# Optimization experiments

Hardware: AMD Instinct MI355X
Metric: run time of the kernel (lower is better)

Reference implementation:

```python
import jax, jax.numpy as jnp
import numpy as np

# Locally-connected 3D conv, channels_last, valid padding, stride 1
B, IX, IY, IZ, CIN = 4, 32, 32, 16, 8
KX, KY, KZ = 3, 3, 3
F = 8
OX, OY, OZ = IX - KX + 1, IY - KY + 1, IZ - KZ + 1  # 30, 30, 14
IN_SIZE = IX * IY * IZ * CIN
OUT_SIZE = OX * OY * OZ * F
NNZ = OX * OY * OZ * F * KX * KY * KZ * CIN  # 21,772,800


def _kernel_idxs():
    # rows/cols of the sparse (OUT_SIZE, IN_SIZE) locally-connected kernel
    # dim order: (ox, oy, oz, fo, kx, ky, kz, ci)
    ox = np.arange(OX).reshape(OX, 1, 1, 1, 1, 1, 1, 1)
    oy = np.arange(OY).reshape(1, OY, 1, 1, 1, 1, 1, 1)
    oz = np.arange(OZ).reshape(1, 1, OZ, 1, 1, 1, 1, 1)
    fo = np.arange(F).reshape(1, 1, 1, F, 1, 1, 1, 1)
    kx = np.arange(KX).reshape(1, 1, 1, 1, KX, 1, 1, 1)
    ky = np.arange(KY).reshape(1, 1, 1, 1, 1, KY, 1, 1)
    kz = np.arange(KZ).reshape(1, 1, 1, 1, 1, 1, KZ, 1)
    ci = np.arange(CIN).reshape(1, 1, 1, 1, 1, 1, 1, CIN)
    full = (OX, OY, OZ, F, KX, KY, KZ, CIN)
    row = ((ox * OY + oy) * OZ + oz) * F + fo
    col = (((ox + kx) * IY + (oy + ky)) * IZ + (oz + kz)) * CIN + ci
    rows = np.broadcast_to(row, full).ravel().astype(np.int32)
    cols = np.broadcast_to(col, full).ravel().astype(np.int32)
    return rows, cols


def setup_inputs() -> dict:
    key = jax.random.key(0)
    k = jax.random.split(key, 7)
    rows, cols = _kernel_idxs()
    inputs = jax.random.normal(k[0], (B, IX, IY, IZ, CIN), dtype=jnp.float32)
    kernel_mean = jax.random.normal(k[1], (NNZ,), dtype=jnp.float32) * 0.05
    # posterior stddev (positive), analogous to softplus(rho) in tfp mean-field posterior
    kernel_std = jax.nn.softplus(jax.random.normal(k[2], (NNZ,), dtype=jnp.float32) - 4.0)
    bias = jax.random.normal(k[3], (OX, OY, OZ, F), dtype=jnp.float32) * 0.05
    eps = jax.random.normal(k[4], (NNZ,), dtype=jnp.float32)
    sign_in = (2.0 * jax.random.bernoulli(k[5], 0.5, (B, IN_SIZE)).astype(jnp.float32) - 1.0)
    sign_out = (2.0 * jax.random.bernoulli(k[6], 0.5, (B, OUT_SIZE)).astype(jnp.float32) - 1.0)
    return {"inputs": inputs, "kernel_mean": kernel_mean, "kernel_std": kernel_std,
            "bias": bias, "eps": eps, "sign_in": sign_in, "sign_out": sign_out,
            "rows": jnp.asarray(rows), "cols": jnp.asarray(cols)}


def _local_conv(x_flat_T, kvals, rows, cols):
    # x_flat_T: [IN_SIZE, B]; sparse matmul: out[row, b] += kvals * x[col, b]
    contrib = kvals[:, None] * x_flat_T[cols]          # [NNZ, B]
    out = jax.ops.segment_sum(contrib, rows, num_segments=OUT_SIZE)  # [OUT_SIZE, B]
    return out.T                                        # [B, OUT_SIZE]


def reference(inputs, kernel_mean, kernel_std, bias, eps, sign_in, sign_out, rows, cols):
    x_flat = inputs.reshape(B, -1)                      # [B, IN_SIZE]
    mean_out = _local_conv(x_flat.T, kernel_mean, rows, cols)
    # flipout perturbation: sign_out * lc(x * sign_in, std * eps)
    pert = _local_conv((x_flat * sign_in).T, kernel_std * eps, rows, cols) * sign_out
    out = (mean_out + pert).reshape(B, OX, OY, OZ, F) + bias
    return out  # linear activation
```

## Files before the change

kernel.cpp:

```cpp
#include <hip/hip_runtime.h>


constexpr int B = 4, IX = 32, IY = 32, IZ = 16, CIN = 8;
constexpr int KX = 3, KY = 3, KZ = 3, F = 8;
constexpr int OX = IX - KX + 1;
constexpr int OY = IY - KY + 1;
constexpr int OZ = IZ - KZ + 1;
constexpr int IN_SIZE  = IX * IY * IZ * CIN;
constexpr int OUT_SIZE = OX * OY * OZ * F;
constexpr int TAPS = KX * KY * KZ * CIN;

__global__ __launch_bounds__(256, 4) void lc3d_flipout_kernel(
    const float* __restrict__ x,
    const float* __restrict__ kmean,
    const float* __restrict__ kstd,
    const float* __restrict__ bias,
    const float* __restrict__ eps,
    const float* __restrict__ sgn_in,
    const float* __restrict__ sgn_out,
    float* __restrict__ out)
{
    const int gtid = blockIdx.x * blockDim.x + threadIdx.x;
    const int o    = gtid >> 6;
    const int lane = threadIdx.x & 63;
    if (o >= OUT_SIZE) return;

    const int t  = o >> 3;
    const int oz = t % OZ;
    const int t2 = t / OZ;
    const int oy = t2 % OY;
    const int ox = t2 / OY;

    float ms0 = 0.f, ms1 = 0.f, ms2 = 0.f, ms3 = 0.f;
    float ps0 = 0.f, ps1 = 0.f, ps2 = 0.f, ps3 = 0.f;

    if (lane < TAPS / 4) {
        const int s   = lane >> 1;
        const int ci0 = (lane & 1) << 2;
        const int kz  = s % KZ;
        const int sy  = s / KZ;
        const int ky  = sy % KY;
        const int kx  = sy / KY;
        const int col = (((ox + kx) * IY + (oy + ky)) * IZ + (oz + kz)) * CIN + ci0;
        const int nb  = o * TAPS + (lane << 2);

        const float4 m4 = *reinterpret_cast<const float4*>(kmean + nb);
        const float4 s4 = *reinterpret_cast<const float4*>(kstd  + nb);
        const float4 e4 = *reinterpret_cast<const float4*>(eps   + nb);
        float4 se;
        se.x = s4.x * e4.x; se.y = s4.y * e4.y; se.z = s4.z * e4.z; se.w = s4.w * e4.w;

#define ACC_BATCH(bi, msv, psv)                                                     \
        {                                                                           \
            const float4 x4 = *reinterpret_cast<const float4*>(x + (bi)*IN_SIZE + col);      \
            const float4 si = *reinterpret_cast<const float4*>(sgn_in + (bi)*IN_SIZE + col); \
            msv += m4.x*x4.x + m4.y*x4.y + m4.z*x4.z + m4.w*x4.w;                   \
            psv += se.x*(x4.x*si.x) + se.y*(x4.y*si.y)                              \
                 + se.z*(x4.z*si.z) + se.w*(x4.w*si.w);                             \
        }
        ACC_BATCH(0, ms0, ps0)
        ACC_BATCH(1, ms1, ps1)
        ACC_BATCH(2, ms2, ps2)
        ACC_BATCH(3, ms3, ps3)
#undef ACC_BATCH
    }

#pragma unroll
    for (int off = 32; off >= 1; off >>= 1) {
        ms0 += __shfl_xor(ms0, off, 64);
        ms1 += __shfl_xor(ms1, off, 64);
        ms2 += __shfl_xor(ms2, off, 64);
        ms3 += __shfl_xor(ms3, off, 64);
        ps0 += __shfl_xor(ps0, off, 64);
        ps1 += __shfl_xor(ps1, off, 64);
        ps2 += __shfl_xor(ps2, off, 64);
        ps3 += __shfl_xor(ps3, off, 64);
    }

    if (lane < B) {
        const float m = (lane == 0) ? ms0 : (lane == 1) ? ms1 : (lane == 2) ? ms2 : ms3;
        const float p = (lane == 0) ? ps0 : (lane == 1) ? ps1 : (lane == 2) ? ps2 : ps3;
        out[lane * OUT_SIZE + o] = m + sgn_out[lane * OUT_SIZE + o] * p + bias[o];
    }
}

extern "C" void kernel_launch(void* const* d_in, const int* in_sizes, int n_in,
                              void* d_out, int out_size, void* d_ws, size_t ws_size,
                              hipStream_t stream) {
    const float* x       = (const float*)d_in[0];
    const float* kmean   = (const float*)d_in[1];
    const float* kstd    = (const float*)d_in[2];
    const float* bias    = (const float*)d_in[3];
    const float* eps     = (const float*)d_in[4];
    const float* sgn_in  = (const float*)d_in[5];
    const float* sgn_out = (const float*)d_in[6];
    float* out = (float*)d_out;

    const int waves   = OUT_SIZE;
    const int threads = 256;
    const int blocks  = (waves * 64 + threads - 1) / threads;

    hipLaunchKernelGGL(lc3d_flipout_kernel, dim3(blocks), dim3(threads), 0, stream,
                       x, kmean, kstd, bias, eps, sgn_in, sgn_out, out);
}
```

Baseline: 343.6 us.

## Map one wavefront per spatial position with all filters and XCD-aware block remap

```diff
diff --git a/kernel.cpp b/kernel.cpp
--- a/kernel.cpp
+++ b/kernel.cpp
@@ -9,8 +9,10 @@
 constexpr int IN_SIZE  = IX * IY * IZ * CIN;
 constexpr int OUT_SIZE = OX * OY * OZ * F;
 constexpr int TAPS = KX * KY * KZ * CIN;
+constexpr int NSPAT = OX * OY * OZ;
+constexpr int WROW = F * TAPS;
 
-__global__ __launch_bounds__(256, 4) void lc3d_flipout_kernel(
+__global__ __launch_bounds__(256, 4) void lc3d_flipout_v2(
     const float* __restrict__ x,
     const float* __restrict__ kmean,
     const float* __restrict__ kstd,
@@ -20,67 +22,74 @@
     const float* __restrict__ sgn_out,
     float* __restrict__ out)
 {
-    const int gtid = blockIdx.x * blockDim.x + threadIdx.x;
-    const int o    = gtid >> 6;
+    const int nwg = (NSPAT * 64) / 256;
+    const int q = nwg / 8, r = nwg % 8;
+    const int xcd = blockIdx.x % 8, idx = blockIdx.x / 8;
+    const int bid = (xcd < r ? xcd * (q + 1) : r * (q + 1) + (xcd - r) * q) + idx;
+
+    const int wid  = (bid * 256 + (int)threadIdx.x) >> 6;
     const int lane = threadIdx.x & 63;
-    if (o >= OUT_SIZE) return;
+    const int fo = lane >> 3;
+    const int g  = lane & 7;
+    const int sp = wid;
+    if (sp >= NSPAT) return;
 
-    const int t  = o >> 3;
-    const int oz = t % OZ;
-    const int t2 = t / OZ;
+    const int oz = sp % OZ;
+    const int t2 = sp / OZ;
     const int oy = t2 % OY;
     const int ox = t2 / OY;
+    const int obase = sp * F;
 
-    float ms0 = 0.f, ms1 = 0.f, ms2 = 0.f, ms3 = 0.f;
-    float ps0 = 0.f, ps1 = 0.f, ps2 = 0.f, ps3 = 0.f;
+    float ms[4] = {0.f, 0.f, 0.f, 0.f};
+    float ps[4] = {0.f, 0.f, 0.f, 0.f};
 
-    if (lane < TAPS / 4) {
-        const int s   = lane >> 1;
-        const int ci0 = (lane & 1) << 2;
-        const int kz  = s % KZ;
-        const int sy  = s / KZ;
-        const int ky  = sy % KY;
-        const int kx  = sy / KY;
-        const int col = (((ox + kx) * IY + (oy + ky)) * IZ + (oz + kz)) * CIN + ci0;
-        const int nb  = o * TAPS + (lane << 2);
+    const int wbase = sp * WROW + fo * TAPS;
 
-        const float4 m4 = *reinterpret_cast<const float4*>(kmean + nb);
-        const float4 s4 = *reinterpret_cast<const float4*>(kstd  + nb);
-        const float4 e4 = *reinterpret_cast<const float4*>(eps   + nb);
-        float4 se;
-        se.x = s4.x * e4.x; se.y = s4.y * e4.y; se.z = s4.z * e4.z; se.w = s4.w * e4.w;
+#pragma unroll
+    for (int j = 0; j < 7; ++j) {
+        const int c = g + 8 * j;
+        if (c < 54) {
+            const int s   = c >> 1;
+            const int ci0 = (c & 1) << 2;
+            const int kz  = s % KZ;
+            const int sy  = s / KZ;
+            const int ky  = sy % KY;
+            const int kx  = sy / KY;
+            const int col = (((ox + kx) * IY + (oy + ky)) * IZ + (oz + kz)) * CIN + ci0;
+            const int nb  = wbase + (c << 2);
 
-#define ACC_BATCH(bi, msv, psv)                                                     \
-        {                                                                           \
-            const float4 x4 = *reinterpret_cast<const float4*>(x + (bi)*IN_SIZE + col);      \
-            const float4 si = *reinterpret_cast<const float4*>(sgn_in + (bi)*IN_SIZE + col); \
-            msv += m4.x*x4.x + m4.y*x4.y + m4.z*x4.z + m4.w*x4.w;                   \
-            psv += se.x*(x4.x*si.x) + se.y*(x4.y*si.y)                              \
-                 + se.z*(x4.z*si.z) + se.w*(x4.w*si.w);                             \
+            const float4 m4 = *reinterpret_cast<const float4*>(kmean + nb);
+            const float4 s4 = *reinterpret_cast<const float4*>(kstd  + nb);
+            const float4 e4 = *reinterpret_cast<const float4*>(eps   + nb);
+            float4 se;
+            se.x = s4.x * e4.x; se.y = s4.y * e4.y;
+            se.z = s4.z * e4.z; se.w = s4.w * e4.w;
+
+#pragma unroll
+            for (int b = 0; b < B; ++b) {
+                const float4 x4 = *reinterpret_cast<const float4*>(x      + b * IN_SIZE + col);
+                const float4 si = *reinterpret_cast<const float4*>(sgn_in + b * IN_SIZE + col);
+                ms[b] += m4.x * x4.x + m4.y * x4.y + m4.z * x4.z + m4.w * x4.w;
+                ps[b] += se.x * (x4.x * si.x) + se.y * (x4.y * si.y)
+                       + se.z * (x4.z * si.z) + se.w * (x4.w * si.w);
+            }
         }
-        ACC_BATCH(0, ms0, ps0)
-        ACC_BATCH(1, ms1, ps1)
-        ACC_BATCH(2, ms2, ps2)
-        ACC_BATCH(3, ms3, ps3)
-#undef ACC_BATCH
     }
 
 #pragma unroll
-    for (int off = 32; off >= 1; off >>= 1) {
-        ms0 += __shfl_xor(ms0, off, 64);
-        ms1 += __shfl_xor(ms1, off, 64);
-        ms2 += __shfl_xor(ms2, off, 64);
-        ms3 += __shfl_xor(ms3, off, 64);
-        ps0 += __shfl_xor(ps0, off, 64);
-        ps1 += __shfl_xor(ps1, off, 64);
-        ps2 += __shfl_xor(ps2, off, 64);
-        ps3 += __shfl_xor(ps3, off, 64);
+    for (int m = 1; m <= 4; m <<= 1) {
+#pragma unroll
+        for (int b = 0; b < B; ++b) {
+            ms[b] += __shfl_xor(ms[b], m, 64);
+            ps[b] += __shfl_xor(ps[b], m, 64);
+        }
     }
 
-    if (lane < B) {
-        const float m = (lane == 0) ? ms0 : (lane == 1) ? ms1 : (lane == 2) ? ms2 : ms3;
-        const float p = (lane == 0) ? ps0 : (lane == 1) ? ps1 : (lane == 2) ? ps2 : ps3;
-        out[lane * OUT_SIZE + o] = m + sgn_out[lane * OUT_SIZE + o] * p + bias[o];
+    if (g < B) {
+        const float m = (g == 0) ? ms[0] : (g == 1) ? ms[1] : (g == 2) ? ms[2] : ms[3];
+        const float p = (g == 0) ? ps[0] : (g == 1) ? ps[1] : (g == 2) ? ps[2] : ps[3];
+        const int o = obase + fo;
+        out[g * OUT_SIZE + o] = m + sgn_out[g * OUT_SIZE + o] * p + bias[o];
     }
 }
 
@@ -96,10 +105,9 @@
     const float* sgn_out = (const float*)d_in[6];
     float* out = (float*)d_out;
 
-    const int waves   = OUT_SIZE;
     const int threads = 256;
-    const int blocks  = (waves * 64 + threads - 1) / threads;
+    const int blocks  = (NSPAT * 64) / threads;
 
-    hipLaunchKernelGGL(lc3d_flipout_kernel, dim3(blocks), dim3(threads), 0, stream,
+    hipLaunchKernelGGL(lc3d_flipout_v2, dim3(blocks), dim3(threads), 0, stream,
                        x, kmean, kstd, bias, eps, sgn_in, sgn_out, out);
 }
```

New measurement: 413.1 us. +20.2%, slower.
